# Kernel tuning notes

Measured on AMD Instinct MI355X. Metric: run time of the kernel, lower is better.

Reference implementation:

```python
import jax, jax.numpy as jnp
import numpy as np

FEAT_BITS = (6, 10)   # (integer bits, fractional bits)
RES_BITS = (6, 10)
DEGREE = 4
N = 4_000_000


def fpq(x, int_bits, frac_bits):
    """Fixed-point quantize: round to 2^-frac_bits grid, clamp to signed range."""
    scale = jnp.float32(2.0 ** frac_bits)
    lo = jnp.float32(-(2.0 ** int_bits))
    hi = jnp.float32(2.0 ** int_bits - 1.0 / (2.0 ** frac_bits))
    return jnp.clip(jnp.round(x * scale) / scale, lo, hi)


def setup_inputs() -> dict:
    key = jax.random.key(0)
    inputs = jax.random.uniform(key, (N, 3), dtype=jnp.float32)
    return {"inputs": inputs}


def reference(inputs):
    fi, ff = FEAT_BITS
    ri, rf = RES_BITS
    x = fpq(inputs[:, 0] * 2 - 1, fi, ff)
    y = fpq(inputs[:, 1] * 2 - 1, fi, ff)
    z = fpq(inputs[:, 2] * 2 - 1, fi, ff)
    xy = fpq(x * y, fi, ff)
    xz = fpq(x * z, fi, ff)
    yz = fpq(y * z, fi, ff)
    x2 = fpq(x * x, fi, ff)
    y2 = fpq(y * y, fi, ff)
    z2 = fpq(z * z, fi, ff)

    def qc(c):  # quantized SH coefficient, as in source
        return fpq(jnp.float32(c), fi, rf)

    def qf(t):  # re-quantize feature (idempotent but faithful)
        return fpq(t, fi, ff)

    def qr(t):  # result quantization
        return fpq(t, ri, rf)

    ones = jnp.ones_like(x)
    cols = []
    # degree >= 1
    cols.append(fpq(jnp.float32(0.28209479177387814), ri, rf) * ones)
    # degree >= 2
    cols.append(qr(qc(-0.48860251190291987) * qf(y)))
    cols.append(qr(qc(0.48860251190291987) * qf(z)))
    cols.append(qr(qc(-0.48860251190291987) * qf(x)))
    # degree >= 3
    cols.append(qr(qc(1.0925484305920792) * qf(xy)))
    cols.append(qr(qc(-1.0925484305920792) * qf(yz)))
    cols.append(qr(qc(0.94617469575756) * qf(z2) - qc(0.31539156525252)))
    cols.append(qr(qc(-1.0925484305920792) * qf(xz)))
    cols.append(qr(qc(0.5462742152960396) * qf(x2) - qc(0.5462742152960396) * qf(y2)))
    # degree >= 4
    cols.append(qr(qc(0.5900435899266435) * qf(y) * qf(-3.0 * x2 + y2)))
    cols.append(qr(qc(2.890611442640554) * qf(xy) * qf(z)))
    cols.append(qr(qc(0.4570457994644657) * qf(y) * qf(1.0 - 5.0 * z2)))
    cols.append(qr(qc(0.3731763325901154) * qf(z) * qf(5.0 * z2 - 3.0)))
    cols.append(qr(qc(0.4570457994644657) * qf(x) * qf(1.0 - 5.0 * z2)))
    cols.append(qr(qc(1.445305721320277) * qf(z) * qf(x2 - y2)))
    cols.append(qr(qc(0.5900435899266435) * qf(x) * qf(-x2 + 3.0 * y2)))

    return jnp.stack(cols, axis=-1)  # [N, 16]
```

## Files before the change

### kernel.cpp

```cpp
#include <hip/hip_runtime.h>

__device__ __forceinline__ float fpq10(float x) {
    float r = rintf(x * 1024.0f) * 0.0009765625f;
    r = fmaxf(r, -64.0f);
    r = fminf(r, 63.9990234375f);
    return r;
}

__global__ __launch_bounds__(256) void qsh_kernel(const float* __restrict__ in,
                                                  float* __restrict__ out,
                                                  int n) {
    int i = blockIdx.x * blockDim.x + threadIdx.x;
    if (i >= n) return;

    size_t b = 3u * (size_t)i;
    float u = in[b + 0];
    float v = in[b + 1];
    float w = in[b + 2];

    float x = fpq10(u * 2.0f - 1.0f);
    float y = fpq10(v * 2.0f - 1.0f);
    float z = fpq10(w * 2.0f - 1.0f);
    float xy = fpq10(x * y);
    float xz = fpq10(x * z);
    float yz = fpq10(y * z);
    float x2 = fpq10(x * x);
    float y2 = fpq10(y * y);
    float z2 = fpq10(z * z);

    const float C0  = 0.2822265625f;
    const float C1  = 0.48828125f;
    const float C2  = 1.0927734375f;
    const float C3  = 0.9462890625f;
    const float C4  = 0.3154296875f;
    const float C5  = 0.5458984375f;
    const float C6  = 0.58984375f;
    const float C7  = 2.890625f;
    const float C8  = 0.45703125f;
    const float C9  = 0.373046875f;
    const float C10 = 1.4453125f;

    float o0  = C0;
    float o1  = fpq10(-C1 * fpq10(y));
    float o2  = fpq10( C1 * fpq10(z));
    float o3  = fpq10(-C1 * fpq10(x));
    float o4  = fpq10( C2 * fpq10(xy));
    float o5  = fpq10(-C2 * fpq10(yz));
    float o6  = fpq10( C3 * fpq10(z2) - C4);
    float o7  = fpq10(-C2 * fpq10(xz));
    float o8  = fpq10( C5 * fpq10(x2) - C5 * fpq10(y2));
    float o9  = fpq10((C6  * fpq10(y)) * fpq10(-3.0f * x2 + y2));
    float o10 = fpq10((C7  * fpq10(xy)) * fpq10(z));
    float o11 = fpq10((C8  * fpq10(y)) * fpq10(1.0f - 5.0f * z2));
    float o12 = fpq10((C9  * fpq10(z)) * fpq10(5.0f * z2 - 3.0f));
    float o13 = fpq10((C8  * fpq10(x)) * fpq10(1.0f - 5.0f * z2));
    float o14 = fpq10((C10 * fpq10(z)) * fpq10(x2 - y2));
    float o15 = fpq10((C6  * fpq10(x)) * fpq10(-x2 + 3.0f * y2));

    float4* op = reinterpret_cast<float4*>(out + (size_t)i * 16);
    op[0] = make_float4(o0,  o1,  o2,  o3);
    op[1] = make_float4(o4,  o5,  o6,  o7);
    op[2] = make_float4(o8,  o9,  o10, o11);
    op[3] = make_float4(o12, o13, o14, o15);
}

extern "C" void kernel_launch(void* const* d_in, const int* in_sizes, int n_in,
                              void* d_out, int out_size, void* d_ws, size_t ws_size,
                              hipStream_t stream) {
    const float* in = (const float*)d_in[0];
    float* out = (float*)d_out;
    int n = in_sizes[0] / 3;
    const int block = 256;
    int grid = (n + block - 1) / block;
    qsh_kernel<<<grid, block, 0, stream>>>(in, out, n);
}
```

Baseline: 305.7 us.

## Stage input and output through LDS for fully coalesced global accesses

Each block now loads its 3-float inputs with contiguous coalesced loads into shared memory and writes its 16 outputs per point into padded shared memory. It then stores them to global memory as consecutive float4s across threads. The aim is to replace the strided per-thread loads and the 64-byte-stride float4 stores with fully contiguous transactions. The cost is two barriers plus the shared-memory traffic.

```diff
diff --git a/kernel.cpp b/kernel.cpp
--- a/kernel.cpp
+++ b/kernel.cpp
@@ -7,16 +7,30 @@
     return r;
 }
 
+#define PTS 256
+#define PAD 20
+
 __global__ __launch_bounds__(256) void qsh_kernel(const float* __restrict__ in,
                                                   float* __restrict__ out,
                                                   int n) {
-    int i = blockIdx.x * blockDim.x + threadIdx.x;
-    if (i >= n) return;
+    __shared__ float s_in[3 * PTS];
+    __shared__ float s_out[PTS * PAD];
 
-    size_t b = 3u * (size_t)i;
-    float u = in[b + 0];
-    float v = in[b + 1];
-    float w = in[b + 2];
+    const int t = threadIdx.x;
+    const long long blockStart = (long long)blockIdx.x * PTS;
+    const long long inBase = blockStart * 3;
+    const long long nIn = (long long)n * 3;
+
+#pragma unroll
+    for (int k = 0; k < 3; ++k) {
+        long long gi = inBase + k * PTS + t;
+        s_in[k * PTS + t] = (gi < nIn) ? in[gi] : 0.0f;
+    }
+    __syncthreads();
+
+    float u = s_in[3 * t + 0];
+    float v = s_in[3 * t + 1];
+    float w = s_in[3 * t + 2];
 
     float x = fpq10(u * 2.0f - 1.0f);
     float y = fpq10(v * 2.0f - 1.0f);
@@ -57,11 +71,26 @@
     float o14 = fpq10((C10 * fpq10(z)) * fpq10(x2 - y2));
     float o15 = fpq10((C6  * fpq10(x)) * fpq10(-x2 + 3.0f * y2));
 
-    float4* op = reinterpret_cast<float4*>(out + (size_t)i * 16);
-    op[0] = make_float4(o0,  o1,  o2,  o3);
-    op[1] = make_float4(o4,  o5,  o6,  o7);
-    op[2] = make_float4(o8,  o9,  o10, o11);
-    op[3] = make_float4(o12, o13, o14, o15);
+    float4* so = reinterpret_cast<float4*>(&s_out[t * PAD]);
+    so[0] = make_float4(o0,  o1,  o2,  o3);
+    so[1] = make_float4(o4,  o5,  o6,  o7);
+    so[2] = make_float4(o8,  o9,  o10, o11);
+    so[3] = make_float4(o12, o13, o14, o15);
+    __syncthreads();
+
+    const long long outBase4 = blockStart * 4;
+    const long long nOut4 = (long long)n * 4;
+    float4* outv = reinterpret_cast<float4*>(out);
+#pragma unroll
+    for (int k = 0; k < 4; ++k) {
+        long long f = outBase4 + k * PTS + t;
+        if (f < nOut4) {
+            int lf = k * PTS + t;
+            int p = lf >> 2;
+            int q = lf & 3;
+            outv[f] = *reinterpret_cast<const float4*>(&s_out[p * PAD + q * 4]);
+        }
+    }
 }
 
 extern "C" void kernel_launch(void* const* d_in, const int* in_sizes, int n_in,
@@ -70,7 +99,6 @@
     const float* in = (const float*)d_in[0];
     float* out = (float*)d_out;
     int n = in_sizes[0] / 3;
-    const int block = 256;
-    int grid = (n + block - 1) / block;
-    qsh_kernel<<<grid, block, 0, stream>>>(in, out, n);
+    int grid = (n + PTS - 1) / PTS;
+    qsh_kernel<<<grid, PTS, 0, stream>>>(in, out, n);
 }
```

Measured after the change: 288.6 us. -5.6%, faster.
